# Kernel tuning notes

Hardware: AMD Instinct MI355X
Metric: run time of the kernel (lower is better)

## Reference

```python
import jax, jax.numpy as jnp
import numpy as np

N, L, CS, CZ, CH, H = 1, 768, 384, 128, 32, 12
EPS = 1e-5


def _layernorm(x, w, b):
    m = jnp.mean(x, axis=-1, keepdims=True)
    v = jnp.mean((x - m) ** 2, axis=-1, keepdims=True)
    return (x - m) * jax.lax.rsqrt(v + EPS) * w + b


def setup_inputs() -> dict:
    key = jax.random.key(0)
    ks = jax.random.split(key, 12)
    scale = 0.02
    return {
        "s": jax.random.normal(ks[0], (N, L, CS), jnp.float32),
        "z": jax.random.normal(ks[1], (N, L, L, CZ), jnp.float32),
        "ln_s_w": jnp.ones((CS,), jnp.float32),
        "ln_s_b": jnp.zeros((CS,), jnp.float32),
        "ln_z_w": jnp.ones((CZ,), jnp.float32),
        "ln_z_b": jnp.zeros((CZ,), jnp.float32),
        "w_z": jax.random.normal(ks[2], (H, CZ), jnp.float32) * scale,   # pair-bias proj (no bias)
        "w_q": jax.random.normal(ks[3], (H * CH, CS), jnp.float32) * scale,
        "w_k": jax.random.normal(ks[4], (H * CH, CS), jnp.float32) * scale,
        "w_v": jax.random.normal(ks[5], (H * CH, CS), jnp.float32) * scale,
        "w_g": jax.random.normal(ks[6], (H * CH, CS), jnp.float32) * scale,
        "b_g": jnp.zeros((H * CH,), jnp.float32),
        "w_o": jax.random.normal(ks[7], (CS, H * CH), jnp.float32) * scale,
        "b_o": jnp.zeros((CS,), jnp.float32),
    }


def reference(s, z, ln_s_w, ln_s_b, ln_z_w, ln_z_b, w_z, w_q, w_k, w_v, w_g, b_g, w_o, b_o):
    s_n = _layernorm(s, ln_s_w, ln_s_b)            # [N,L,CS]
    z_n = _layernorm(z, ln_z_w, ln_z_b)            # [N,L,L,CZ]
    # pair bias: Linear(c_z -> H, bias=False), then permute to [N,H,L,L]
    bias = jnp.einsum("nijc,hc->nhij", z_n, w_z)   # [N,H,L,L]
    # AF2-style gated MHA on s
    q = jnp.einsum("nlc,dc->nld", s_n, w_q).reshape(N, L, H, CH) * (CH ** -0.5)
    k = jnp.einsum("nlc,dc->nld", s_n, w_k).reshape(N, L, H, CH)
    v = jnp.einsum("nlc,dc->nld", s_n, w_v).reshape(N, L, H, CH)
    logits = jnp.einsum("nqhc,nkhc->nhqk", q, k) + bias
    a = jax.nn.softmax(logits, axis=-1)
    o = jnp.einsum("nhqk,nkhc->nqhc", a, v).reshape(N, L, H * CH)
    g = jax.nn.sigmoid(jnp.einsum("nlc,dc->nld", s_n, w_g) + b_g)
    o = o * g
    return jnp.einsum("nld,cd->nlc", o, w_o) + b_o  # [N,L,CS]
```

## Files before the change

kernel.cpp:

```cpp
#include <hip/hip_runtime.h>
#include <hip/hip_bf16.h>
#include <cstddef>

#define L_ 768
#define CS_ 384
#define CZ_ 128
#define CH_ 32
#define H_ 12
#define LL_ (L_*L_)
#define EPS_ 1e-5f

typedef float f4 __attribute__((ext_vector_type(4)));

__global__ void prep_kernel(const float* __restrict__ lnzw, const float* __restrict__ lnzb,
                            const float* __restrict__ wz,
                            float* __restrict__ ww, float* __restrict__ sumww,
                            float* __restrict__ bb) {
    int h = threadIdx.x;
    if (h < H_) {
        float sw = 0.f, sb = 0.f;
        for (int c = 0; c < CZ_; ++c) {
            float wv = lnzw[c] * wz[h*CZ_ + c];
            ww[h*CZ_ + c] = wv;
            sw += wv;
            sb += lnzb[c] * wz[h*CZ_ + c];
        }
        sumww[h] = sw;
        bb[h] = sb;
    }
}

__global__ __launch_bounds__(128) void bias_kernel(const float* __restrict__ z,
        const float* __restrict__ ww, const float* __restrict__ sumww,
        const float* __restrict__ bb, float* __restrict__ bias) {
    __shared__ float zb[2][256][36];
    __shared__ float lw[H_*CZ_];
    __shared__ float lsw[H_];
    __shared__ float lbb[H_];

    const int t  = threadIdx.x;
    const size_t tb = (size_t)blockIdx.x * 256;
    const int sr = t >> 3;
    const int s8 = t & 7;

    const f4* zf4 = (const f4*)z;

    f4 st[16];
    #pragma unroll
    for (int p = 0; p < 16; ++p)
        st[p] = __builtin_nontemporal_load(&zf4[(tb + p*16 + sr)*32 + s8]);

    {
        const f4* wwf4 = (const f4*)ww;
        f4* lwf4 = (f4*)lw;
        #pragma unroll
        for (int i = 0; i < 3; ++i) lwf4[i*128 + t] = wwf4[i*128 + t];
        if (t < H_) { lsw[t] = sumww[t]; lbb[t] = bb[t]; }
    }

    float acc0[H_], acc1[H_];
    #pragma unroll
    for (int h = 0; h < H_; ++h) { acc0[h] = 0.f; acc1[h] = 0.f; }
    float s0 = 0.f, q0 = 0.f, s1 = 0.f, q1 = 0.f;

    #pragma unroll 1
    for (int c = 0; c < 4; ++c) {
        #pragma unroll
        for (int p = 0; p < 16; ++p)
            *(f4*)&zb[c&1][p*16 + sr][s8*4] = st[p];
        if (c < 3) {
            #pragma unroll
            for (int p = 0; p < 16; ++p)
                st[p] = __builtin_nontemporal_load(&zf4[(tb + p*16 + sr)*32 + (c+1)*8 + s8]);
        }
        __syncthreads();

        #pragma unroll
        for (int j = 0; j < 8; ++j) {
            f4 z0 = *(const f4*)&zb[c&1][t][j*4];
            f4 z1 = *(const f4*)&zb[c&1][t+128][j*4];
            s0 += z0.x+z0.y+z0.z+z0.w;
            q0 += z0.x*z0.x+z0.y*z0.y+z0.z*z0.z+z0.w*z0.w;
            s1 += z1.x+z1.y+z1.z+z1.w;
            q1 += z1.x*z1.x+z1.y*z1.y+z1.z*z1.z+z1.w*z1.w;
            const int cb = c*32 + j*4;
            #pragma unroll
            for (int h = 0; h < H_; ++h) {
                f4 wv = *(const f4*)&lw[h*CZ_ + cb];
                acc0[h] += z0.x*wv.x + z0.y*wv.y + z0.z*wv.z + z0.w*wv.w;
                acc1[h] += z1.x*wv.x + z1.y*wv.y + z1.z*wv.z + z1.w*wv.w;
            }
        }
        __syncthreads();
    }

    float m0 = s0 * (1.f/CZ_);
    float r0 = rsqrtf(q0*(1.f/CZ_) - m0*m0 + EPS_);
    float m1 = s1 * (1.f/CZ_);
    float r1 = rsqrtf(q1*(1.f/CZ_) - m1*m1 + EPS_);
    #pragma unroll
    for (int h = 0; h < H_; ++h) {
        bias[(size_t)h*LL_ + tb + t]       = r0*(acc0[h] - m0*lsw[h]) + lbb[h];
        bias[(size_t)h*LL_ + tb + 128 + t] = r1*(acc1[h] - m1*lsw[h]) + lbb[h];
    }
}

__global__ void sln_kernel(const float* __restrict__ s, const float* __restrict__ w,
                           const float* __restrict__ b, float* __restrict__ sn) {
    int row = blockIdx.x;
    int lane = threadIdx.x;
    float x[6];
    float sum = 0.f, sum2 = 0.f;
    #pragma unroll
    for (int j = 0; j < 6; ++j) {
        x[j] = s[row*CS_ + lane + j*64];
        sum += x[j]; sum2 += x[j]*x[j];
    }
    #pragma unroll
    for (int off = 32; off; off >>= 1) {
        sum  += __shfl_xor(sum,  off);
        sum2 += __shfl_xor(sum2, off);
    }
    float m = sum * (1.f/CS_);
    float r = rsqrtf(sum2*(1.f/CS_) - m*m + EPS_);
    #pragma unroll
    for (int j = 0; j < 6; ++j) {
        int c = lane + j*64;
        sn[row*CS_ + c] = (x[j]-m)*r*w[c] + b[c];
    }
}

__global__ __launch_bounds__(256) void qkvg_kernel(const float* __restrict__ sn,
        const float* __restrict__ wq, const float* __restrict__ wk,
        const float* __restrict__ wv, const float* __restrict__ wg,
        const float* __restrict__ bg,
        float* __restrict__ qb, float* __restrict__ kb,
        float* __restrict__ vb, float* __restrict__ gb) {
    __shared__ float As[16][68];
    __shared__ float Bs[16][68];
    int m0 = blockIdx.x * 64;
    int n0 = blockIdx.y * 64;
    int sel = n0 / 384;
    const float* W = (sel==0) ? wq : (sel==1) ? wk : (sel==2) ? wv : wg;
    float* C       = (sel==0) ? qb : (sel==1) ? kb : (sel==2) ? vb : gb;
    int ncol0 = n0 - sel*384;

    int t  = threadIdx.x;
    int lr = t >> 2;
    int lc = (t & 3) * 4;
    int ty = t >> 4;
    int tx = t & 15;

    float acc[4][4] = {};
    for (int k0 = 0; k0 < CS_; k0 += 16) {
        float4 av = *(const float4*)(sn + (size_t)(m0 + lr)*CS_ + k0 + lc);
        float4 bv = *(const float4*)(W  + (size_t)(ncol0 + lr)*CS_ + k0 + lc);
        As[lc+0][lr] = av.x; As[lc+1][lr] = av.y; As[lc+2][lr] = av.z; As[lc+3][lr] = av.w;
        Bs[lc+0][lr] = bv.x; Bs[lc+1][lr] = bv.y; Bs[lc+2][lr] = bv.z; Bs[lc+3][lr] = bv.w;
        __syncthreads();
        #pragma unroll
        for (int kk = 0; kk < 16; ++kk) {
            float4 a4 = *(const float4*)&As[kk][ty*4];
            float4 b4 = *(const float4*)&Bs[kk][tx*4];
            float a[4] = {a4.x,a4.y,a4.z,a4.w};
            float bb_[4] = {b4.x,b4.y,b4.z,b4.w};
            #pragma unroll
            for (int i = 0; i < 4; ++i)
                #pragma unroll
                for (int j = 0; j < 4; ++j)
                    acc[i][j] += a[i]*bb_[j];
        }
        __syncthreads();
    }
    #pragma unroll
    for (int i = 0; i < 4; ++i) {
        int row = m0 + ty*4 + i;
        #pragma unroll
        for (int j = 0; j < 4; ++j) {
            int col = ncol0 + tx*4 + j;
            float v = acc[i][j];
            if (sel == 0) v *= 0.17677669529663687f;
            if (sel == 3) v = 1.f/(1.f + __expf(-(v + bg[col])));
            C[(size_t)row*CS_ + col] = v;
        }
    }
}

#define QT_ 8
__global__ __launch_bounds__(256) void attn_kernel(const float* __restrict__ qb,
        const float* __restrict__ kb, const float* __restrict__ vb,
        const float* __restrict__ gb, const float* __restrict__ bias,
        float* __restrict__ og) {
    __shared__ float Sm[QT_][772];
    __shared__ float KVt[CH_][136];
    int h  = blockIdx.x;
    int q0 = blockIdx.y * QT_;
    int t  = threadIdx.x;

    int tq = t >> 5;
    int tk = t & 31;

    float qreg[CH_];
    {
        const float4* qsrc = (const float4*)(qb + (size_t)(q0 + tq)*CS_ + h*CH_);
        #pragma unroll
        for (int i = 0; i < 8; ++i) {
            float4 qv = qsrc[i];
            qreg[i*4+0]=qv.x; qreg[i*4+1]=qv.y; qreg[i*4+2]=qv.z; qreg[i*4+3]=qv.w;
        }
    }

    for (int kt = 0; kt < L_; kt += 128) {
        #pragma unroll
        for (int r2 = 0; r2 < 4; ++r2) {
            int row = (t >> 3) + 32*r2;
            int c   = (t & 7) * 4;
            f4 kv = *(const f4*)(kb + (size_t)(kt+row)*CS_ + h*CH_ + c);
            KVt[c+0][row]=kv.x; KVt[c+1][row]=kv.y; KVt[c+2][row]=kv.z; KVt[c+3][row]=kv.w;
        }
        __syncthreads();
        f4 sacc = {0,0,0,0};
        #pragma unroll
        for (int c = 0; c < CH_; ++c) {
            f4 kv4 = *(const f4*)&KVt[c][tk*4];
            sacc.x += qreg[c]*kv4.x;
            sacc.y += qreg[c]*kv4.y;
            sacc.z += qreg[c]*kv4.z;
            sacc.w += qreg[c]*kv4.w;
        }
        f4 bv = *(const f4*)(bias + (size_t)h*LL_ + (size_t)(q0+tq)*L_ + kt + tk*4);
        *(f4*)&Sm[tq][kt + tk*4] = sacc + bv;
        __syncthreads();
    }

    {
        float mx = -1e30f;
        for (int k = tk; k < L_; k += 32) mx = fmaxf(mx, Sm[tq][k]);
        #pragma unroll
        for (int off = 16; off; off >>= 1) mx = fmaxf(mx, __shfl_xor(mx, off));
        float ssum = 0.f;
        for (int k = tk; k < L_; k += 32) {
            float e = __expf(Sm[tq][k] - mx);
            Sm[tq][k] = e;
            ssum += e;
        }
        #pragma unroll
        for (int off = 16; off; off >>= 1) ssum += __shfl_xor(ssum, off);
        float inv = 1.f/ssum;
        for (int k = tk; k < L_; k += 32) Sm[tq][k] *= inv;
        __syncthreads();
    }

    {
        float o = 0.f;
        for (int kt = 0; kt < L_; kt += 128) {
            #pragma unroll
            for (int r2 = 0; r2 < 4; ++r2) {
                int row = (t >> 3) + 32*r2;
                int c   = (t & 7) * 4;
                f4 vv = *(const f4*)(vb + (size_t)(kt+row)*CS_ + h*CH_ + c);
                KVt[c+0][row]=vv.x; KVt[c+1][row]=vv.y; KVt[c+2][row]=vv.z; KVt[c+3][row]=vv.w;
            }
            __syncthreads();
            #pragma unroll
            for (int j4 = 0; j4 < 32; ++j4) {
                f4 pv = *(const f4*)&Sm[tq][kt + j4*4];
                f4 va = *(const f4*)&KVt[tk][j4*4];
                o += pv.x*va.x + pv.y*va.y + pv.z*va.z + pv.w*va.w;
            }
            __syncthreads();
        }
        int row = q0 + tq;
        int c   = h*CH_ + tk;
        og[(size_t)row*CS_ + c] = o * gb[(size_t)row*CS_ + c];
    }
}

__global__ __launch_bounds__(256) void outproj_kernel(const float* __restrict__ og,
        const float* __restrict__ wo, const float* __restrict__ bo,
        float* __restrict__ out) {
    __shared__ float As[16][68];
    __shared__ float Bs[16][68];
    int m0 = blockIdx.x * 64;
    int n0 = blockIdx.y * 64;
    int t  = threadIdx.x;
    int lr = t >> 2;
    int lc = (t & 3) * 4;
    int ty = t >> 4;
    int tx = t & 15;
    float acc[4][4] = {};
    for (int k0 = 0; k0 < CS_; k0 += 16) {
        float4 av = *(const float4*)(og + (size_t)(m0 + lr)*CS_ + k0 + lc);
        float4 bv = *(const float4*)(wo + (size_t)(n0 + lr)*CS_ + k0 + lc);
        As[lc+0][lr] = av.x; As[lc+1][lr] = av.y; As[lc+2][lr] = av.z; As[lc+3][lr] = av.w;
        Bs[lc+0][lr] = bv.x; Bs[lc+1][lr] = bv.y; Bs[lc+2][lr] = bv.z; Bs[lc+3][lr] = bv.w;
        __syncthreads();
        #pragma unroll
        for (int kk = 0; kk < 16; ++kk) {
            float4 a4 = *(const float4*)&As[kk][ty*4];
            float4 b4 = *(const float4*)&Bs[kk][tx*4];
            float a[4] = {a4.x,a4.y,a4.z,a4.w};
            float bb_[4] = {b4.x,b4.y,b4.z,b4.w};
            #pragma unroll
            for (int i = 0; i < 4; ++i)
                #pragma unroll
                for (int j = 0; j < 4; ++j)
                    acc[i][j] += a[i]*bb_[j];
        }
        __syncthreads();
    }
    #pragma unroll
    for (int i = 0; i < 4; ++i) {
        int row = m0 + ty*4 + i;
        #pragma unroll
        for (int j = 0; j < 4; ++j) {
            int col = n0 + tx*4 + j;
            out[(size_t)row*CS_ + col] = acc[i][j] + bo[col];
        }
    }
}

extern "C" void kernel_launch(void* const* d_in, const int* in_sizes, int n_in,
                              void* d_out, int out_size, void* d_ws, size_t ws_size,
                              hipStream_t stream) {
    const float* s      = (const float*)d_in[0];
    const float* z      = (const float*)d_in[1];
    const float* ln_s_w = (const float*)d_in[2];
    const float* ln_s_b = (const float*)d_in[3];
    const float* ln_z_w = (const float*)d_in[4];
    const float* ln_z_b = (const float*)d_in[5];
    const float* w_z    = (const float*)d_in[6];
    const float* w_q    = (const float*)d_in[7];
    const float* w_k    = (const float*)d_in[8];
    const float* w_v    = (const float*)d_in[9];
    const float* w_g    = (const float*)d_in[10];
    const float* b_g    = (const float*)d_in[11];
    const float* w_o    = (const float*)d_in[12];
    const float* b_o    = (const float*)d_in[13];
    float* out = (float*)d_out;

    float* ws    = (float*)d_ws;
    float* bias  = ws;
    float* sn    = bias + (size_t)H_*LL_;
    float* qb    = sn + (size_t)L_*CS_;
    float* kb    = qb + (size_t)L_*CS_;
    float* vb    = kb + (size_t)L_*CS_;
    float* gb    = vb + (size_t)L_*CS_;
    float* og    = gb + (size_t)L_*CS_;
    float* ww    = og + (size_t)L_*CS_;
    float* sumww = ww + (size_t)H_*CZ_;
    float* bbuf  = sumww + 16;

    hipLaunchKernelGGL(prep_kernel, dim3(1), dim3(64), 0, stream,
                       ln_z_w, ln_z_b, w_z, ww, sumww, bbuf);
    hipLaunchKernelGGL(bias_kernel, dim3(LL_/256), dim3(128), 0, stream,
                       z, ww, sumww, bbuf, bias);
    hipLaunchKernelGGL(sln_kernel, dim3(L_), dim3(64), 0, stream,
                       s, ln_s_w, ln_s_b, sn);
    hipLaunchKernelGGL(qkvg_kernel, dim3(L_/64, 1536/64), dim3(256), 0, stream,
                       sn, w_q, w_k, w_v, w_g, b_g, qb, kb, vb, gb);
    hipLaunchKernelGGL(attn_kernel, dim3(H_, L_/QT_), dim3(256), 0, stream,
                       qb, kb, vb, gb, bias, og);
    hipLaunchKernelGGL(outproj_kernel, dim3(L_/64, CS_/64), dim3(256), 0, stream,
                       og, w_o, b_o, out);
}
```

Before: 209.9 us.

## Retile bias kernel per thread over rows and heads; shrink outproj tiles

The bias kernel now has each thread handle 4 consecutive rows and 6 of the 12 heads instead of 2 rows and all heads. Each weight vector loaded from LDS is reused across 4 rows, and the bias output is written as float4 vectors. The output projection moves from 64x64 to 32x32 tiles, giving 4x more blocks to occupy more CUs at the cost of less reuse per block. The new LDS read pattern (row stride 36 floats across lanes) and the duplicated LayerNorm statistics across the two head groups may add bank conflicts and redundant work.

```diff
diff --git a/kernel.cpp b/kernel.cpp
--- a/kernel.cpp
+++ b/kernel.cpp
@@ -11,6 +11,7 @@
 #define EPS_ 1e-5f
 
 typedef float f4 __attribute__((ext_vector_type(4)));
+typedef float f2 __attribute__((ext_vector_type(2)));
 
 __global__ void prep_kernel(const float* __restrict__ lnzw, const float* __restrict__ lnzb,
                             const float* __restrict__ wz,
@@ -33,7 +34,7 @@
 __global__ __launch_bounds__(128) void bias_kernel(const float* __restrict__ z,
         const float* __restrict__ ww, const float* __restrict__ sumww,
         const float* __restrict__ bb, float* __restrict__ bias) {
-    __shared__ float zb[2][256][36];
+    __shared__ float zb[2][256*36];
     __shared__ float lw[H_*CZ_];
     __shared__ float lsw[H_];
     __shared__ float lbb[H_];
@@ -42,6 +43,8 @@
     const size_t tb = (size_t)blockIdx.x * 256;
     const int sr = t >> 3;
     const int s8 = t & 7;
+    const int rg = t & 63;
+    const int hg = t >> 6;
 
     const f4* zf4 = (const f4*)z;
 
@@ -58,16 +61,18 @@
         if (t < H_) { lsw[t] = sumww[t]; lbb[t] = bb[t]; }
     }
 
-    float acc0[H_], acc1[H_];
-    #pragma unroll
-    for (int h = 0; h < H_; ++h) { acc0[h] = 0.f; acc1[h] = 0.f; }
-    float s0 = 0.f, q0 = 0.f, s1 = 0.f, q1 = 0.f;
+    float acc[6][4];
+    #pragma unroll
+    for (int h = 0; h < 6; ++h)
+        #pragma unroll
+        for (int i = 0; i < 4; ++i) acc[h][i] = 0.f;
+    float sm[4] = {0,0,0,0}, sq[4] = {0,0,0,0};
 
     #pragma unroll 1
     for (int c = 0; c < 4; ++c) {
         #pragma unroll
         for (int p = 0; p < 16; ++p)
-            *(f4*)&zb[c&1][p*16 + sr][s8*4] = st[p];
+            *(f4*)&zb[c&1][(p*16 + sr)*36 + s8*4] = st[p];
         if (c < 3) {
             #pragma unroll
             for (int p = 0; p < 16; ++p)
@@ -77,31 +82,43 @@
 
         #pragma unroll
         for (int j = 0; j < 8; ++j) {
-            f4 z0 = *(const f4*)&zb[c&1][t][j*4];
-            f4 z1 = *(const f4*)&zb[c&1][t+128][j*4];
-            s0 += z0.x+z0.y+z0.z+z0.w;
-            q0 += z0.x*z0.x+z0.y*z0.y+z0.z*z0.z+z0.w*z0.w;
-            s1 += z1.x+z1.y+z1.z+z1.w;
-            q1 += z1.x*z1.x+z1.y*z1.y+z1.z*z1.z+z1.w*z1.w;
+            f4 zv[4];
+            #pragma unroll
+            for (int i = 0; i < 4; ++i)
+                zv[i] = *(const f4*)&zb[c&1][(rg*4 + i)*36 + j*4];
+            #pragma unroll
+            for (int i = 0; i < 4; ++i) {
+                sm[i] += zv[i].x + zv[i].y + zv[i].z + zv[i].w;
+                sq[i] += zv[i].x*zv[i].x + zv[i].y*zv[i].y + zv[i].z*zv[i].z + zv[i].w*zv[i].w;
+            }
             const int cb = c*32 + j*4;
             #pragma unroll
-            for (int h = 0; h < H_; ++h) {
-                f4 wv = *(const f4*)&lw[h*CZ_ + cb];
-                acc0[h] += z0.x*wv.x + z0.y*wv.y + z0.z*wv.z + z0.w*wv.w;
-                acc1[h] += z1.x*wv.x + z1.y*wv.y + z1.z*wv.z + z1.w*wv.w;
+            for (int h = 0; h < 6; ++h) {
+                f4 wv = *(const f4*)&lw[(hg*6 + h)*CZ_ + cb];
+                #pragma unroll
+                for (int i = 0; i < 4; ++i)
+                    acc[h][i] += zv[i].x*wv.x + zv[i].y*wv.y + zv[i].z*wv.z + zv[i].w*wv.w;
             }
         }
         __syncthreads();
     }
 
-    float m0 = s0 * (1.f/CZ_);
-    float r0 = rsqrtf(q0*(1.f/CZ_) - m0*m0 + EPS_);
-    float m1 = s1 * (1.f/CZ_);
-    float r1 = rsqrtf(q1*(1.f/CZ_) - m1*m1 + EPS_);
-    #pragma unroll
-    for (int h = 0; h < H_; ++h) {
-        bias[(size_t)h*LL_ + tb + t]       = r0*(acc0[h] - m0*lsw[h]) + lbb[h];
-        bias[(size_t)h*LL_ + tb + 128 + t] = r1*(acc1[h] - m1*lsw[h]) + lbb[h];
+    float mm[4], rr[4];
+    #pragma unroll
+    for (int i = 0; i < 4; ++i) {
+        mm[i] = sm[i] * (1.f/CZ_);
+        rr[i] = rsqrtf(sq[i]*(1.f/CZ_) - mm[i]*mm[i] + EPS_);
+    }
+    #pragma unroll
+    for (int h = 0; h < 6; ++h) {
+        const int hh = hg*6 + h;
+        const float sw = lsw[hh], bbv = lbb[hh];
+        f4 o;
+        o.x = rr[0]*(acc[h][0] - mm[0]*sw) + bbv;
+        o.y = rr[1]*(acc[h][1] - mm[1]*sw) + bbv;
+        o.z = rr[2]*(acc[h][2] - mm[2]*sw) + bbv;
+        o.w = rr[3]*(acc[h][3] - mm[3]*sw) + bbv;
+        *(f4*)(bias + (size_t)hh*LL_ + tb + rg*4) = o;
     }
 }
 
@@ -279,42 +296,39 @@
 __global__ __launch_bounds__(256) void outproj_kernel(const float* __restrict__ og,
         const float* __restrict__ wo, const float* __restrict__ bo,
         float* __restrict__ out) {
-    __shared__ float As[16][68];
-    __shared__ float Bs[16][68];
-    int m0 = blockIdx.x * 64;
-    int n0 = blockIdx.y * 64;
+    __shared__ float As[16][36];
+    __shared__ float Bs[16][36];
+    int m0 = blockIdx.x * 32;
+    int n0 = blockIdx.y * 32;
     int t  = threadIdx.x;
-    int lr = t >> 2;
-    int lc = (t & 3) * 4;
+    int lr = t >> 3;
+    int lc = (t & 7) * 2;
     int ty = t >> 4;
     int tx = t & 15;
-    float acc[4][4] = {};
+    float acc[2][2] = {};
     for (int k0 = 0; k0 < CS_; k0 += 16) {
-        float4 av = *(const float4*)(og + (size_t)(m0 + lr)*CS_ + k0 + lc);
-        float4 bv = *(const float4*)(wo + (size_t)(n0 + lr)*CS_ + k0 + lc);
-        As[lc+0][lr] = av.x; As[lc+1][lr] = av.y; As[lc+2][lr] = av.z; As[lc+3][lr] = av.w;
-        Bs[lc+0][lr] = bv.x; Bs[lc+1][lr] = bv.y; Bs[lc+2][lr] = bv.z; Bs[lc+3][lr] = bv.w;
+        f2 av = *(const f2*)(og + (size_t)(m0 + lr)*CS_ + k0 + lc);
+        f2 bv = *(const f2*)(wo + (size_t)(n0 + lr)*CS_ + k0 + lc);
+        As[lc+0][lr] = av.x; As[lc+1][lr] = av.y;
+        Bs[lc+0][lr] = bv.x; Bs[lc+1][lr] = bv.y;
         __syncthreads();
         #pragma unroll
         for (int kk = 0; kk < 16; ++kk) {
-            float4 a4 = *(const float4*)&As[kk][ty*4];
-            float4 b4 = *(const float4*)&Bs[kk][tx*4];
-            float a[4] = {a4.x,a4.y,a4.z,a4.w};
-            float bb_[4] = {b4.x,b4.y,b4.z,b4.w};
-            #pragma unroll
-            for (int i = 0; i < 4; ++i)
-                #pragma unroll
-                for (int j = 0; j < 4; ++j)
-                    acc[i][j] += a[i]*bb_[j];
-        }
-        __syncthreads();
-    }
-    #pragma unroll
-    for (int i = 0; i < 4; ++i) {
-        int row = m0 + ty*4 + i;
-        #pragma unroll
-        for (int j = 0; j < 4; ++j) {
-            int col = n0 + tx*4 + j;
+            f2 a2 = *(const f2*)&As[kk][ty*2];
+            f2 b2 = *(const f2*)&Bs[kk][tx*2];
+            acc[0][0] += a2.x*b2.x;
+            acc[0][1] += a2.x*b2.y;
+            acc[1][0] += a2.y*b2.x;
+            acc[1][1] += a2.y*b2.y;
+        }
+        __syncthreads();
+    }
+    #pragma unroll
+    for (int i = 0; i < 2; ++i) {
+        int row = m0 + ty*2 + i;
+        #pragma unroll
+        for (int j = 0; j < 2; ++j) {
+            int col = n0 + tx*2 + j;
             out[(size_t)row*CS_ + col] = acc[i][j] + bo[col];
         }
     }
@@ -361,6 +375,6 @@
                        sn, w_q, w_k, w_v, w_g, b_g, qb, kb, vb, gb);
     hipLaunchKernelGGL(attn_kernel, dim3(H_, L_/QT_), dim3(256), 0, stream,
                        qb, kb, vb, gb, bias, og);
-    hipLaunchKernelGGL(outproj_kernel, dim3(L_/64, CS_/64), dim3(256), 0, stream,
+    hipLaunchKernelGGL(outproj_kernel, dim3(L_/32, CS_/32), dim3(256), 0, stream,
                        og, w_o, b_o, out);
 }
```

New measurement: 209.1 us. No clear change (-0.4%).
